# Optimization experiments

Measured on AMD Instinct MI355X. Metric: run time of the kernel, lower is better.

## Reference

```python
import jax, jax.numpy as jnp
import numpy as np

N = 100000
E = 1250000
D = 64
R = 16


def _glorot(key, shape):
    fan_in, fan_out = shape[-2], shape[-1]
    lim = jnp.sqrt(6.0 / (fan_in + fan_out))
    return jax.random.uniform(key, shape, jnp.float32, -lim, lim)


def setup_inputs() -> dict:
    key = jax.random.key(0)
    ks = jax.random.split(key, 9)
    x = jax.random.normal(ks[0], (N, D), jnp.float32)
    edge_index = jax.random.randint(ks[1], (2, E), 0, N, jnp.int64 if jax.config.jax_enable_x64 else jnp.int32).astype(jnp.int32)
    edge_type = jax.random.randint(ks[2], (E,), 0, R).astype(jnp.int32)
    return {
        "x": x,
        "edge_index": edge_index,
        "edge_type": edge_type,
        "W1": _glorot(ks[3], (R, D, D)),
        "sw1": _glorot(ks[4], (D, D)),
        "b1": jnp.zeros((D,), jnp.float32),
        "W2": _glorot(ks[5], (R, D, D)),
        "sw2": _glorot(ks[6], (D, D)),
        "b2": jnp.zeros((D,), jnp.float32),
    }


def _rgcn_layer(x, src, dst, edge_type, W, sw, b, residual):
    # self transform [N, O]
    out = x @ sw
    # per-relation transform of all nodes: [N, R, O] (avoids [E, D, O] gathered weights,
    # same math as bmm(x_j, W[edge_type]))
    xW = jnp.einsum('nd,rdo->nro', x, W)
    msg = xW[src, edge_type]                      # [E, O] per-edge messages
    agg = jax.ops.segment_sum(msg, dst, num_segments=N)  # scatter-add aggregate
    out = out + agg
    if residual:
        out = out + x  # Identity residual (in == out channels)
    out = out + b
    return jax.nn.relu(out)


def reference(x, edge_index, edge_type, W1, sw1, b1, W2, sw2, b2):
    src, dst = edge_index[0], edge_index[1]
    # layer 1: residual=True; layer 2: encoding=False -> no residual.
    # activation (relu) applied after every layer by RGCN.forward; dropout p=0 / eval -> no-op.
    h = _rgcn_layer(x, src, dst, edge_type, W1, sw1, b1, residual=True)
    h = _rgcn_layer(h, src, dst, edge_type, W2, sw2, b2, residual=False)
    return h
```

## Files before the change

kernel.cpp:

```cpp
#include <hip/hip_runtime.h>
#include <hip/hip_bf16.h>

#define NN 100000
#define NE 1250000
#define DD 64
#define RR 16
#define NTILE 6250
#define NBINS 100000
#define NBLK_SCAN 391
#define EBCAP 512

typedef __attribute__((ext_vector_type(8))) short s16x8;
typedef __attribute__((ext_vector_type(4))) float f32x4;

static __device__ __forceinline__ unsigned short f2bf(float v) {
    __hip_bfloat16 h = __float2bfloat16(v);
    return __builtin_bit_cast(unsigned short, h);
}
static __device__ __forceinline__ unsigned int pack2(float a, float b) {
    return ((unsigned int)f2bf(b) << 16) | (unsigned int)f2bf(a);
}


__global__ void hist_key(const int* __restrict__ dst, const int* __restrict__ et,
                         int* __restrict__ cnt) {
    int e = blockIdx.x * 256 + threadIdx.x;
    if (e < NE) atomicAdd(&cnt[(dst[e] >> 4) * 16 + et[e]], 1);
}

__global__ __launch_bounds__(256) void scan1(const int* __restrict__ cnt,
                                             int* __restrict__ rp, int* __restrict__ part) {
    __shared__ int s[256];
    int i = blockIdx.x * 256 + threadIdx.x;
    int v = (i < NBINS) ? cnt[i] : 0;
    s[threadIdx.x] = v;
    __syncthreads();
    for (int off = 1; off < 256; off <<= 1) {
        int t = (threadIdx.x >= off) ? s[threadIdx.x - off] : 0;
        __syncthreads();
        s[threadIdx.x] += t;
        __syncthreads();
    }
    if (i < NBINS) rp[i] = s[threadIdx.x] - v;
    if (threadIdx.x == 255) part[blockIdx.x] = s[255];
}

__global__ void scan2(int* __restrict__ part, int* __restrict__ rp) {
    __shared__ int s[NBLK_SCAN];
    if (threadIdx.x < NBLK_SCAN) s[threadIdx.x] = part[threadIdx.x];
    __syncthreads();
    if (threadIdx.x == 0) {
        int acc = 0;
        for (int b = 0; b < NBLK_SCAN; ++b) { int t = s[b]; s[b] = acc; acc += t; }
        rp[NBINS] = NE;
    }
    __syncthreads();
    if (threadIdx.x < NBLK_SCAN) part[threadIdx.x] = s[threadIdx.x];
}

__global__ void scan3(int* __restrict__ rp, const int* __restrict__ part, int* __restrict__ cur) {
    int i = blockIdx.x * 256 + threadIdx.x;
    if (i < NBINS) {
        int v = rp[i] + part[blockIdx.x];
        rp[i] = v;
        cur[i] = v;
    }
}

__global__ void scatter_key(const int* __restrict__ src, const int* __restrict__ dst,
                            const int* __restrict__ et, int* __restrict__ cur,
                            unsigned int* __restrict__ ep) {
    int e = blockIdx.x * 256 + threadIdx.x;
    if (e >= NE) return;
    int d = dst[e];
    int p = atomicAdd(&cur[(d >> 4) * 16 + et[e]], 1);
    ep[p] = (unsigned int)src[e] | ((unsigned int)(d & 15) << 20);
}


__global__ void prep_w2(const float* __restrict__ W1, const float* __restrict__ sw1,
                        const float* __restrict__ W2, const float* __restrict__ sw2,
                        unsigned short* __restrict__ wt) {
    int i = blockIdx.x * 256 + threadIdx.x;
    if (i >= 2 * 17 * DD * DD) return;
    int d = i & 63;
    int o = (i >> 6) & 63;
    int p = (i >> 12) % 17;
    int l = i / (17 * DD * DD);
    const float* srcp;
    if (p < 16) srcp = (l ? W2 : W1) + p * DD * DD;
    else        srcp = (l ? sw2 : sw1);
    wt[i] = f2bf(srcp[d * DD + o]);
}

__global__ void prep_x2(const float* __restrict__ x, unsigned short* __restrict__ xb) {
    int i = blockIdx.x * blockDim.x + threadIdx.x;
    if (i < NN * DD) xb[i] = f2bf(x[i]);
}

__global__ __launch_bounds__(256) void fused_layer(
    const unsigned short* __restrict__ xb,
    const unsigned short* __restrict__ wt,
    const int* __restrict__ rp,
    const unsigned int* __restrict__ ep,
    const float* __restrict__ bias,
    const float* __restrict__ xres,
    unsigned short* __restrict__ outb,
    float* __restrict__ outf)
{
    __shared__ unsigned int eb[EBCAP];
    __shared__ int rps[17];
    __shared__ float Dred[4 * 1024];
    const int tid  = threadIdx.x;
    const int wid  = tid >> 6;
    const int lane = tid & 63;
    const int c = lane & 15;
    const int q = lane >> 4;
    const int tile = blockIdx.x;
    const int n0 = tile * 16;

    if (tid < 17) rps[tid] = rp[tile * 16 + tid];
    __syncthreads();
    const int e0 = rps[0];
    const int cntT = rps[16] - e0;
    const bool inLds = (cntT <= EBCAP);
    const int nst = min(cntT, EBCAP);
    for (int i = tid; i < nst; i += 256) eb[i] = ep[e0 + i];
    __syncthreads();

    f32x4 D[4];
    #pragma unroll
    for (int ob = 0; ob < 4; ++ob) D[ob] = (f32x4){0.f, 0.f, 0.f, 0.f};

    for (int r = wid; r < 17; r += 4) {
        const unsigned short* wp = wt + r * (DD * DD);
        int s0, s1;
        if (r < 16) { s0 = rps[r]; s1 = rps[r + 1]; } else { s0 = 0; s1 = 16; }

        for (int b0 = s0; b0 < s1; b0 += 32) {
            const int rem = s1 - b0;
            int srcA, dlA;
            if (r < 16) {
                int eA = min(b0 + c, s1 - 1);
                unsigned int wa = inLds ? eb[eA - e0] : ep[eA];
                srcA = (int)(wa & 0xFFFFF);
                dlA  = (b0 + c < s1) ? (int)(wa >> 20) : 31;
            } else { srcA = n0 + c; dlA = c; }
            const bool hasB = (rem > 16);
            int srcB = srcA, dlB = 31;
            if (hasB) {
                int eB = min(b0 + 16 + c, s1 - 1);
                unsigned int wb = inLds ? eb[eB - e0] : ep[eB];
                srcB = (int)(wb & 0xFFFFF);
                dlB  = (b0 + 16 + c < s1) ? (int)(wb >> 20) : 31;
            }

            const unsigned short* xrA = xb + (size_t)srcA * DD + q * 8;
            s16x8 aA0 = *(const s16x8*)(xrA);
            s16x8 aA1 = *(const s16x8*)(xrA + 32);
            s16x8 aB0, aB1;
            if (hasB) {
                const unsigned short* xrB = xb + (size_t)srcB * DD + q * 8;
                aB0 = *(const s16x8*)(xrB);
                aB1 = *(const s16x8*)(xrB + 32);
            }

            s16x8 a2;
            #pragma unroll
            for (int j = 0; j < 4; ++j) {
                int dj = __shfl(dlA, q * 4 + j, 64);
                a2[j] = (dj == c) ? (short)0x3F80 : (short)0;
            }
            if (hasB) {
                #pragma unroll
                for (int j = 0; j < 4; ++j) {
                    int dj = __shfl(dlB, q * 4 + j, 64);
                    a2[j + 4] = (dj == c) ? (short)0x3F80 : (short)0;
                }
            } else {
                #pragma unroll
                for (int j = 0; j < 4; ++j) a2[j + 4] = 0;
            }

            #pragma unroll
            for (int ob = 0; ob < 4; ++ob) {
                const unsigned short* wrow = wp + (ob * 16 + c) * DD + q * 8;
                s16x8 w0 = *(const s16x8*)(wrow);
                s16x8 w1 = *(const s16x8*)(wrow + 32);
                f32x4 cA = {0.f, 0.f, 0.f, 0.f};
                cA = __builtin_amdgcn_mfma_f32_16x16x32_bf16(aA0, w0, cA, 0, 0, 0);
                cA = __builtin_amdgcn_mfma_f32_16x16x32_bf16(aA1, w1, cA, 0, 0, 0);
                s16x8 b2;
                if (hasB) {
                    f32x4 cB = {0.f, 0.f, 0.f, 0.f};
                    cB = __builtin_amdgcn_mfma_f32_16x16x32_bf16(aB0, w0, cB, 0, 0, 0);
                    cB = __builtin_amdgcn_mfma_f32_16x16x32_bf16(aB1, w1, cB, 0, 0, 0);
                    #pragma unroll
                    for (int j = 0; j < 4; ++j) {
                        b2[j]     = (short)f2bf(cA[j]);
                        b2[j + 4] = (short)f2bf(cB[j]);
                    }
                } else {
                    #pragma unroll
                    for (int j = 0; j < 4; ++j) {
                        b2[j]     = (short)f2bf(cA[j]);
                        b2[j + 4] = 0;
                    }
                }
                D[ob] = __builtin_amdgcn_mfma_f32_16x16x32_bf16(a2, b2, D[ob], 0, 0, 0);
            }
        }
    }

    {
        float* dred = Dred + wid * 1024;
        #pragma unroll
        for (int ob = 0; ob < 4; ++ob)
            #pragma unroll
            for (int v = 0; v < 4; ++v)
                dred[(q * 4 + v) * 64 + ob * 16 + c] = D[ob][v];
    }
    __syncthreads();

    #pragma unroll
    for (int k = 0; k < 2; ++k) {
        int j = k * 512 + tid * 2;
        int node = j >> 6, ch = j & 63;
        float v0 = Dred[j]        + Dred[1024 + j]     + Dred[2048 + j]     + Dred[3072 + j];
        float v1 = Dred[j + 1]    + Dred[1024 + j + 1] + Dred[2048 + j + 1] + Dred[3072 + j + 1];
        v0 += bias[ch];
        v1 += bias[ch + 1];
        if (xres) {
            const float2 rv = *(const float2*)(xres + (size_t)(n0 + node) * DD + ch);
            v0 += rv.x; v1 += rv.y;
        }
        v0 = fmaxf(v0, 0.f);
        v1 = fmaxf(v1, 0.f);
        if (outb)
            *(unsigned int*)(outb + (size_t)(n0 + node) * DD + ch) = pack2(v0, v1);
        if (outf) {
            float2 o = {v0, v1};
            *(float2*)(outf + (size_t)(n0 + node) * DD + ch) = o;
        }
    }
}


extern "C" void kernel_launch(void* const* d_in, const int* in_sizes, int n_in,
                              void* d_out, int out_size, void* d_ws, size_t ws_size,
                              hipStream_t stream)
{
    (void)in_sizes; (void)n_in; (void)out_size; (void)ws_size;
    const float* x    = (const float*)d_in[0];
    const int*   ei   = (const int*)d_in[1];
    const int*   et   = (const int*)d_in[2];
    const float* W1   = (const float*)d_in[3];
    const float* sw1  = (const float*)d_in[4];
    const float* b1   = (const float*)d_in[5];
    const float* W2   = (const float*)d_in[6];
    const float* sw2  = (const float*)d_in[7];
    const float* b2   = (const float*)d_in[8];
    float* out = (float*)d_out;

    const int* srcA = ei;
    const int* dstA = ei + NE;

    char* ws = (char*)d_ws;
    unsigned short* xb   = (unsigned short*)(ws);
    unsigned short* h1b  = (unsigned short*)(ws + 12800000);
    unsigned short* wt2  = (unsigned short*)(ws + 25600000);
    unsigned int*   ep   = (unsigned int*)(ws + 25878528);
    int*            rp   = (int*)(ws + 30878528);
    int*            cnt  = (int*)(ws + 31278544);
    int*            cur  = (int*)(ws + 31678544);
    int*            part = (int*)(ws + 32078544);

    const int NB_E    = (NE + 255) / 256;
    const int NB_ELEM = (NN * DD + 255) / 256;
    const int WPL = 17 * DD * DD;

    hipMemsetAsync(cnt, 0, NBINS * sizeof(int), stream);
    hist_key<<<NB_E, 256, 0, stream>>>(dstA, et, cnt);
    scan1<<<NBLK_SCAN, 256, 0, stream>>>(cnt, rp, part);
    scan2<<<1, 512, 0, stream>>>(part, rp);
    scan3<<<NBLK_SCAN, 256, 0, stream>>>(rp, part, cur);
    scatter_key<<<NB_E, 256, 0, stream>>>(srcA, dstA, et, cur, ep);

    prep_w2<<<(2 * 17 * DD * DD + 255) / 256, 256, 0, stream>>>(W1, sw1, W2, sw2, wt2);
    prep_x2<<<NB_ELEM, 256, 0, stream>>>(x, xb);

    fused_layer<<<NTILE, 256, 0, stream>>>(xb, wt2, rp, ep, b1, x, h1b, nullptr);
    fused_layer<<<NTILE, 256, 0, stream>>>(h1b, wt2 + WPL, rp, ep, b2, nullptr, nullptr, out);
}
```

Baseline: 489.3 us.

## Split output channels across waves and stage gathered source rows in LDS

The fused layer now gives each wave one 16-channel output slice across all relations, where before each wave handled a subset of relations for all 64 channels and the four partial results were reduced through LDS. Gathered source rows of x for up to 256 edges per tile are staged once in padded LDS rows and shared by all four waves. Destination indices are kept as bytes in LDS. Each wave prefetches the next relation's weights and raises its scheduling priority around the MFMA block. The aim is to drop the repeated global gathers and the cross-wave reduction, at the cost of every wave walking all 16 relations with a serial loop and extra masking logic.

```diff
diff --git a/kernel.cpp b/kernel.cpp
--- a/kernel.cpp
+++ b/kernel.cpp
@@ -8,7 +8,9 @@
 #define NTILE 6250
 #define NBINS 100000
 #define NBLK_SCAN 391
-#define EBCAP 512
+#define CAPROWS 256
+#define ROWB 144
+#define DLCAP 576
 
 typedef __attribute__((ext_vector_type(8))) short s16x8;
 typedef __attribute__((ext_vector_type(4))) float f32x4;
@@ -98,7 +100,7 @@
     if (i < NN * DD) xb[i] = f2bf(x[i]);
 }
 
-__global__ __launch_bounds__(256) void fused_layer(
+__global__ __launch_bounds__(256, 4) void fused_layer(
     const unsigned short* __restrict__ xb,
     const unsigned short* __restrict__ wt,
     const int* __restrict__ rp,
@@ -108,9 +110,9 @@
     unsigned short* __restrict__ outb,
     float* __restrict__ outf)
 {
-    __shared__ unsigned int eb[EBCAP];
-    __shared__ int rps[17];
-    __shared__ float Dred[4 * 1024];
+    __shared__ __attribute__((aligned(16))) unsigned char Ash[CAPROWS * ROWB];
+    __shared__ __attribute__((aligned(8)))  unsigned char dlb[DLCAP + 32];
+
     const int tid  = threadIdx.x;
     const int wid  = tid >> 6;
     const int lane = tid & 63;
@@ -119,128 +121,173 @@
     const int tile = blockIdx.x;
     const int n0 = tile * 16;
 
-    if (tid < 17) rps[tid] = rp[tile * 16 + tid];
+    const int e0  = rp[tile * 16];
+    const int cnt = rp[tile * 16 + 16] - e0;
+
+    {
+        const int lim = cnt < DLCAP ? cnt : DLCAP;
+        for (int i = tid; i < lim; i += 256)
+            dlb[i] = (unsigned char)(ep[e0 + i] >> 20);
+        if (tid < 32) {
+            int p = lim + tid;
+            if (p < DLCAP + 32) dlb[p] = 0xFF;
+        }
+    }
+    {
+        const int nrows = cnt < CAPROWS ? cnt : CAPROWS;
+        const int half = tid & 1;
+        for (int i = tid >> 1; i < nrows; i += 128) {
+            int src = (int)(ep[e0 + i] & 0xFFFFF);
+            const unsigned short* xr = xb + (size_t)src * DD + half * 32;
+            s16x8 v0 = *(const s16x8*)(xr);
+            s16x8 v1 = *(const s16x8*)(xr + 8);
+            s16x8 v2 = *(const s16x8*)(xr + 16);
+            s16x8 v3 = *(const s16x8*)(xr + 24);
+            unsigned char* bp = Ash + i * ROWB + half * 64;
+            *(s16x8*)(bp)      = v0;
+            *(s16x8*)(bp + 16) = v1;
+            *(s16x8*)(bp + 32) = v2;
+            *(s16x8*)(bp + 48) = v3;
+        }
+    }
     __syncthreads();
-    const int e0 = rps[0];
-    const int cntT = rps[16] - e0;
-    const bool inLds = (cntT <= EBCAP);
-    const int nst = min(cntT, EBCAP);
-    for (int i = tid; i < nst; i += 256) eb[i] = ep[e0 + i];
-    __syncthreads();
-
-    f32x4 D[4];
-    #pragma unroll
-    for (int ob = 0; ob < 4; ++ob) D[ob] = (f32x4){0.f, 0.f, 0.f, 0.f};
-
-    for (int r = wid; r < 17; r += 4) {
-        const unsigned short* wp = wt + r * (DD * DD);
-        int s0, s1;
-        if (r < 16) { s0 = rps[r]; s1 = rps[r + 1]; } else { s0 = 0; s1 = 16; }
-
+
+    const bool dlOK = (cnt <= DLCAP);
+    const int och = wid * 16 + c;
+    const unsigned short* wbase = wt + (size_t)och * DD + q * 8;
+    s16x8 w0 = *(const s16x8*)(wbase);
+    s16x8 w1 = *(const s16x8*)(wbase + 32);
+    f32x4 Dacc = {0.f, 0.f, 0.f, 0.f};
+    const short one = (short)0x3F80;
+
+    for (int r = 0; r < 16; ++r) {
+        const unsigned short* nwp = wbase + (size_t)(r + 1) * (DD * DD);
+        s16x8 nw0 = *(const s16x8*)(nwp);
+        s16x8 nw1 = *(const s16x8*)(nwp + 32);
+
+        const int s0 = rp[tile * 16 + r];
+        const int s1 = rp[tile * 16 + r + 1];
         for (int b0 = s0; b0 < s1; b0 += 32) {
             const int rem = s1 - b0;
-            int srcA, dlA;
-            if (r < 16) {
+            const bool hasB = (rem > 16);
+            const int lbase = b0 - e0;
+
+            s16x8 a2;
+            if (dlOK) {
+                const unsigned* dl32 = (const unsigned*)dlb;
+                int idx = lbase + q * 4;
+                int w = idx >> 2;
+                int sh = (idx & 3) * 8;
+                unsigned long long pa =
+                    ((unsigned long long)dl32[w + 1] << 32) | dl32[w];
+                unsigned da = (unsigned)(pa >> sh);
+                unsigned db = 0;
+                if (hasB) {
+                    unsigned long long pb =
+                        ((unsigned long long)dl32[w + 5] << 32) | dl32[w + 4];
+                    db = (unsigned)(pb >> sh);
+                }
+                #pragma unroll
+                for (int j = 0; j < 4; ++j) {
+                    int jj = q * 4 + j;
+                    a2[j]     = ((int)((da >> (8 * j)) & 255) == c && jj < rem)
+                                ? one : (short)0;
+                    a2[j + 4] = (hasB && (int)((db >> (8 * j)) & 255) == c && jj < rem - 16)
+                                ? one : (short)0;
+                }
+            } else {
                 int eA = min(b0 + c, s1 - 1);
-                unsigned int wa = inLds ? eb[eA - e0] : ep[eA];
-                srcA = (int)(wa & 0xFFFFF);
-                dlA  = (b0 + c < s1) ? (int)(wa >> 20) : 31;
-            } else { srcA = n0 + c; dlA = c; }
-            const bool hasB = (rem > 16);
-            int srcB = srcA, dlB = 31;
-            if (hasB) {
-                int eB = min(b0 + 16 + c, s1 - 1);
-                unsigned int wb = inLds ? eb[eB - e0] : ep[eB];
-                srcB = (int)(wb & 0xFFFFF);
-                dlB  = (b0 + 16 + c < s1) ? (int)(wb >> 20) : 31;
+                unsigned wa = ep[eA];
+                int dlA = (b0 + c < s1) ? (int)(wa >> 20) : 31;
+                int dlB = 31;
+                if (hasB) {
+                    int eB = min(b0 + 16 + c, s1 - 1);
+                    unsigned wb = ep[eB];
+                    dlB = (b0 + 16 + c < s1) ? (int)(wb >> 20) : 31;
+                }
+                #pragma unroll
+                for (int j = 0; j < 4; ++j) {
+                    int dj = __shfl(dlA, q * 4 + j, 64);
+                    a2[j] = (dj == c) ? one : (short)0;
+                    int djb = __shfl(dlB, q * 4 + j, 64);
+                    a2[j + 4] = (hasB && djb == c) ? one : (short)0;
+                }
             }
 
-            const unsigned short* xrA = xb + (size_t)srcA * DD + q * 8;
-            s16x8 aA0 = *(const s16x8*)(xrA);
-            s16x8 aA1 = *(const s16x8*)(xrA + 32);
+            int rA = min(b0 + c, s1 - 1) - e0;
+            s16x8 aA0, aA1;
+            if (rA < CAPROWS) {
+                const unsigned char* ap = Ash + rA * ROWB + q * 16;
+                aA0 = *(const s16x8*)(ap);
+                aA1 = *(const s16x8*)(ap + 64);
+            } else {
+                int srcA = (int)(ep[e0 + rA] & 0xFFFFF);
+                const unsigned short* xr = xb + (size_t)srcA * DD + q * 8;
+                aA0 = *(const s16x8*)(xr);
+                aA1 = *(const s16x8*)(xr + 32);
+            }
             s16x8 aB0, aB1;
             if (hasB) {
-                const unsigned short* xrB = xb + (size_t)srcB * DD + q * 8;
-                aB0 = *(const s16x8*)(xrB);
-                aB1 = *(const s16x8*)(xrB + 32);
+                int rB = min(b0 + 16 + c, s1 - 1) - e0;
+                if (rB < CAPROWS) {
+                    const unsigned char* bp = Ash + rB * ROWB + q * 16;
+                    aB0 = *(const s16x8*)(bp);
+                    aB1 = *(const s16x8*)(bp + 64);
+                } else {
+                    int srcB = (int)(ep[e0 + rB] & 0xFFFFF);
+                    const unsigned short* xr = xb + (size_t)srcB * DD + q * 8;
+                    aB0 = *(const s16x8*)(xr);
+                    aB1 = *(const s16x8*)(xr + 32);
+                }
             }
 
-            s16x8 a2;
-            #pragma unroll
-            for (int j = 0; j < 4; ++j) {
-                int dj = __shfl(dlA, q * 4 + j, 64);
-                a2[j] = (dj == c) ? (short)0x3F80 : (short)0;
-            }
+            __builtin_amdgcn_s_setprio(1);
+            f32x4 cA = {0.f, 0.f, 0.f, 0.f};
+            cA = __builtin_amdgcn_mfma_f32_16x16x32_bf16(aA0, w0, cA, 0, 0, 0);
+            cA = __builtin_amdgcn_mfma_f32_16x16x32_bf16(aA1, w1, cA, 0, 0, 0);
+            s16x8 b2v;
             if (hasB) {
+                f32x4 cB = {0.f, 0.f, 0.f, 0.f};
+                cB = __builtin_amdgcn_mfma_f32_16x16x32_bf16(aB0, w0, cB, 0, 0, 0);
+                cB = __builtin_amdgcn_mfma_f32_16x16x32_bf16(aB1, w1, cB, 0, 0, 0);
                 #pragma unroll
                 for (int j = 0; j < 4; ++j) {
-                    int dj = __shfl(dlB, q * 4 + j, 64);
-                    a2[j + 4] = (dj == c) ? (short)0x3F80 : (short)0;
+                    b2v[j]     = (short)f2bf(cA[j]);
+                    b2v[j + 4] = (short)f2bf(cB[j]);
                 }
             } else {
                 #pragma unroll
-                for (int j = 0; j < 4; ++j) a2[j + 4] = 0;
+                for (int j = 0; j < 4; ++j) {
+                    b2v[j]     = (short)f2bf(cA[j]);
+                    b2v[j + 4] = 0;
+                }
             }
-
-            #pragma unroll
-            for (int ob = 0; ob < 4; ++ob) {
-                const unsigned short* wrow = wp + (ob * 16 + c) * DD + q * 8;
-                s16x8 w0 = *(const s16x8*)(wrow);
-                s16x8 w1 = *(const s16x8*)(wrow + 32);
-                f32x4 cA = {0.f, 0.f, 0.f, 0.f};
-                cA = __builtin_amdgcn_mfma_f32_16x16x32_bf16(aA0, w0, cA, 0, 0, 0);
-                cA = __builtin_amdgcn_mfma_f32_16x16x32_bf16(aA1, w1, cA, 0, 0, 0);
-                s16x8 b2;
-                if (hasB) {
-                    f32x4 cB = {0.f, 0.f, 0.f, 0.f};
-                    cB = __builtin_amdgcn_mfma_f32_16x16x32_bf16(aB0, w0, cB, 0, 0, 0);
-                    cB = __builtin_amdgcn_mfma_f32_16x16x32_bf16(aB1, w1, cB, 0, 0, 0);
-                    #pragma unroll
-                    for (int j = 0; j < 4; ++j) {
-                        b2[j]     = (short)f2bf(cA[j]);
-                        b2[j + 4] = (short)f2bf(cB[j]);
-                    }
-                } else {
-                    #pragma unroll
-                    for (int j = 0; j < 4; ++j) {
-                        b2[j]     = (short)f2bf(cA[j]);
-                        b2[j + 4] = 0;
-                    }
-                }
-                D[ob] = __builtin_amdgcn_mfma_f32_16x16x32_bf16(a2, b2, D[ob], 0, 0, 0);
-            }
+            Dacc = __builtin_amdgcn_mfma_f32_16x16x32_bf16(a2, b2v, Dacc, 0, 0, 0);
+            __builtin_amdgcn_s_setprio(0);
         }
+        w0 = nw0; w1 = nw1;
     }
 
     {
-        float* dred = Dred + wid * 1024;
-        #pragma unroll
-        for (int ob = 0; ob < 4; ++ob)
-            #pragma unroll
-            for (int v = 0; v < 4; ++v)
-                dred[(q * 4 + v) * 64 + ob * 16 + c] = D[ob][v];
-    }
-    __syncthreads();
-
+        const unsigned short* xr = xb + (size_t)(n0 + c) * DD + q * 8;
+        s16x8 a0 = *(const s16x8*)(xr);
+        s16x8 a1 = *(const s16x8*)(xr + 32);
+        Dacc = __builtin_amdgcn_mfma_f32_16x16x32_bf16(a0, w0, Dacc, 0, 0, 0);
+        Dacc = __builtin_amdgcn_mfma_f32_16x16x32_bf16(a1, w1, Dacc, 0, 0, 0);
+    }
+
+    const float bc = bias[och];
     #pragma unroll
-    for (int k = 0; k < 2; ++k) {
-        int j = k * 512 + tid * 2;
-        int node = j >> 6, ch = j & 63;
-        float v0 = Dred[j]        + Dred[1024 + j]     + Dred[2048 + j]     + Dred[3072 + j];
-        float v1 = Dred[j + 1]    + Dred[1024 + j + 1] + Dred[2048 + j + 1] + Dred[3072 + j + 1];
-        v0 += bias[ch];
-        v1 += bias[ch + 1];
-        if (xres) {
-            const float2 rv = *(const float2*)(xres + (size_t)(n0 + node) * DD + ch);
-            v0 += rv.x; v1 += rv.y;
-        }
-        v0 = fmaxf(v0, 0.f);
-        v1 = fmaxf(v1, 0.f);
-        if (outb)
-            *(unsigned int*)(outb + (size_t)(n0 + node) * DD + ch) = pack2(v0, v1);
-        if (outf) {
-            float2 o = {v0, v1};
-            *(float2*)(outf + (size_t)(n0 + node) * DD + ch) = o;
+    for (int v = 0; v < 4; ++v) {
+        const int node = n0 + q * 4 + v;
+        float val = Dacc[v] + bc;
+        if (xres) val += xres[(size_t)node * DD + och];
+        val = fmaxf(val, 0.f);
+        if (outf) outf[(size_t)node * DD + och] = val;
+        if (outb) {
+            float nb = __shfl_xor(val, 1, 64);
+            if (!(c & 1))
+                *(unsigned int*)(outb + (size_t)node * DD + och) = pack2(val, nb);
         }
     }
 }
```

After: 554.0 us. +13.2%, slower.
